# Kernel optimization log

Measured on AMD Instinct MI355X. Metric: run time of the kernel, lower is better.

The kernel has to match this reference:

```python
import jax, jax.numpy as jnp
import numpy as np

BN_EPS = 1e-5
LEAKY_SLOPE = 0.2


def setup_inputs() -> dict:
    key = jax.random.key(0)
    k1, k2 = jax.random.split(key, 2)
    B, C, N, O, K = 8, 64, 4096, 64, 20
    x = jax.random.normal(k1, (B, C, N), dtype=jnp.float32)
    W = jax.random.normal(k2, (O, 2 * C), dtype=jnp.float32) * 0.05  # 1x1 conv weight
    gamma = jnp.ones((O,), dtype=jnp.float32)
    beta = jnp.zeros((O,), dtype=jnp.float32)
    return {"x": x, "W": W, "gamma": gamma, "beta": beta, "k": K}


def reference(x, W, gamma, beta, k):
    # x: (B, C, N)
    xt = jnp.transpose(x, (0, 2, 1))  # (B, N, C)
    # kNN via squared euclidean distances (same ordering as cdist p=2)
    sq = jnp.sum(xt * xt, axis=-1)  # (B, N)
    d2 = sq[:, :, None] + sq[:, None, :] - 2.0 * jnp.einsum('bnc,bmc->bnm', xt, xt)
    idx = jax.lax.top_k(-d2, k)[1]  # (B, N, k) nearest neighbors (incl. self)
    # gather neighbor features: (B, N, k, C)
    xj = jax.vmap(lambda f, i: f[i])(xt, idx)
    xi = xt[:, :, None, :]  # (B, N, 1, C)
    edge = jnp.concatenate([xj - xi, jnp.broadcast_to(xi, xj.shape)], axis=-1)  # (B, N, k, 2C)
    # 1x1 conv == channel GEMM
    h = jnp.einsum('bnkc,oc->bnko', edge, W)  # (B, N, k, O)
    # BatchNorm2d, training-mode batch statistics over (B, N, k) per channel
    mean = jnp.mean(h, axis=(0, 1, 2))
    var = jnp.mean(jnp.square(h - mean), axis=(0, 1, 2))
    hn = (h - mean) * jax.lax.rsqrt(var + BN_EPS) * gamma + beta
    # LeakyReLU(0.2); dropout omitted (eval / identity)
    act = jnp.where(hn >= 0, hn, LEAKY_SLOPE * hn)
    # max over the k neighbors -> (B, N, O) -> (B, O, N)
    out = jnp.max(act, axis=2)
    return jnp.transpose(out, (0, 2, 1))
```

## Files before the change

### kernel.cpp

```cpp
#include <hip/hip_runtime.h>
#include <math.h>

#define Bn 8
#define Cc 64
#define Nn 4096
#define Oo 64
#define Kk 20
#define Kh 10
#define QCAP 16
#define NTOT (Bn*Nn*Kk)

typedef __attribute__((ext_vector_type(8))) short short8;
typedef __attribute__((ext_vector_type(4))) float f32x4;

__device__ __forceinline__ unsigned bf16_rn(float v) {
  unsigned u = __float_as_uint(v);
  return (u + 0x7FFFu + ((u >> 16) & 1)) >> 16;
}

__device__ __forceinline__ float pair_swap_f(float v) {
  return __int_as_float(__builtin_amdgcn_mov_dpp(__float_as_int(v), 0xB1, 0xF, 0xF, true));
}
__device__ __forceinline__ int pair_swap_i(int v) {
  return __builtin_amdgcn_mov_dpp(v, 0xB1, 0xF, 0xF, true);
}

__global__ __launch_bounds__(256) void k_split(const float* __restrict__ x,
                                               unsigned short* __restrict__ xs3,
                                               float* __restrict__ sqv) {
  __shared__ float xs[64][68];
  int tid = threadIdx.x;
  int b = blockIdx.x & 7;
  int n0 = (blockIdx.x >> 3) << 6;
  for (int i = 0; i < 4; i++) {
    int c = i * 16 + (tid >> 4);
    int n = (tid & 15) * 4;
    float4 v = *(const float4*)&x[((size_t)b * Cc + c) * Nn + n0 + n];
    *(float4*)&xs[c][n] = v;
  }
  __syncthreads();
  for (int i = 0; i < 4; i++) {
    int n = i * 16 + (tid >> 4);
    int c = (tid & 15) * 4;
    ushort4 h4, m4, l4;
    unsigned short* hp = (unsigned short*)&h4;
    unsigned short* mp = (unsigned short*)&m4;
    unsigned short* lp = (unsigned short*)&l4;
#pragma unroll
    for (int j = 0; j < 4; j++) {
      float v = xs[c + j][n];
      unsigned hb = bf16_rn(v);
      float hf = __uint_as_float(hb << 16);
      float r1 = v - hf;
      unsigned mb = bf16_rn(r1);
      float mf = __uint_as_float(mb << 16);
      float r2 = r1 - mf;
      unsigned lb = bf16_rn(r2);
      hp[j] = (unsigned short)hb;
      mp[j] = (unsigned short)mb;
      lp[j] = (unsigned short)lb;
    }
    size_t o = ((size_t)(b << 12) + n0 + n) * 192 + c;
    *(ushort4*)&xs3[o] = h4;
    *(ushort4*)&xs3[o + 64] = m4;
    *(ushort4*)&xs3[o + 128] = l4;
  }
  if (tid < 64) {
    float s = 0.f;
#pragma unroll
    for (int c = 0; c < 64; c++) { float v = xs[c][tid]; s = fmaf(v, v, s); }
    sqv[b * Nn + n0 + tid] = s;
  }
}

__global__ __launch_bounds__(256) void k_y1z(const float* __restrict__ x,
                                             const float* __restrict__ Wm,
                                             float* __restrict__ y1,
                                             float* __restrict__ z) {
  __shared__ float xs[64][68];
  __shared__ float Wl[64][129];
  int tid = threadIdx.x;
  int b = blockIdx.x & 7;
  int n0 = (blockIdx.x >> 3) << 6;
  for (int i = tid; i < 64 * 128; i += 256) Wl[i >> 7][i & 127] = Wm[i];
  for (int i = 0; i < 4; i++) {
    int c = i * 16 + (tid >> 4);
    int n = (tid & 15) * 4;
    float4 v = *(const float4*)&x[((size_t)b * Cc + c) * Nn + n0 + n];
    *(float4*)&xs[c][n] = v;
  }
  __syncthreads();
  int o = tid & 63, ng = tid >> 6;
  for (int p = 0; p < 4; p++) {
    int nb = p * 16 + ng * 4;
    float a1[4] = {0.f, 0.f, 0.f, 0.f};
    float a2[4] = {0.f, 0.f, 0.f, 0.f};
#pragma unroll 8
    for (int c = 0; c < 64; c++) {
      float4 xv = *(const float4*)&xs[c][nb];
      float w1v = Wl[o][c], w2v = Wl[o][64 + c];
      float xa[4] = {xv.x, xv.y, xv.z, xv.w};
#pragma unroll
      for (int j = 0; j < 4; j++) {
        a1[j] = fmaf(xa[j], w1v, a1[j]);
        a2[j] = fmaf(xa[j], w2v, a2[j]);
      }
    }
#pragma unroll
    for (int j = 0; j < 4; j++) {
      size_t off = ((size_t)b * Nn + n0 + nb + j) * 64 + o;
      y1[off] = a1[j];
      z[off] = a2[j] - a1[j];
    }
  }
}

__global__ __launch_bounds__(512, 4) void k_knn(const unsigned short* __restrict__ xs3,
                                                const float* __restrict__ sqv,
                                                int* __restrict__ idxout) {
  __shared__ alignas(16) short Bs[2][3][64][72];
  __shared__ float thrS[2][64];
  __shared__ float sqs[2][64];
  __shared__ alignas(16) float qk[2][64][20];
  __shared__ alignas(16) unsigned short qm[2][64][24];
  __shared__ int qcnt[2][64];

  const int tid = threadIdx.x;
  const int lane = tid & 63;
  const int w = tid >> 6;
  const int grp = w >> 2;
  const int wg = w & 3;
  const int tig = tid & 255;
  const int b = blockIdx.x & 7;
  const int n0 = (blockIdx.x >> 3) << 6;
  const int lm = lane & 15;
  const int q = lane >> 4;
  const bool handler = (lane < 32);
  const int hrow = wg * 16 + (lane >> 1);
  const bool isL = (lane & 1) == 0;

  float hk[Kh];
  int hix[Kh];
#pragma unroll
  for (int kk = 0; kk < Kh; kk++) { hk[kk] = INFINITY; hix[kk] = 0; }

  if (handler && !isL) { thrS[grp][hrow] = INFINITY; qcnt[grp][hrow] = 0; }

  const size_t arow = ((size_t)(b << 12) + n0 + wg * 16 + lm) * 192;
  short8 ah0 = *(const short8*)&xs3[arow + q * 8];
  short8 ah1 = *(const short8*)&xs3[arow + 32 + q * 8];
  short8 am0 = *(const short8*)&xs3[arow + 64 + q * 8];
  short8 am1 = *(const short8*)&xs3[arow + 96 + q * 8];
  short8 al0 = *(const short8*)&xs3[arow + 128 + q * 8];
  short8 al1 = *(const short8*)&xs3[arow + 160 + q * 8];

  const unsigned short* gp = xs3 + ((size_t)(b << 12) + grp * 2048) * 192 + tig * 8;
  short* ld[6];
#pragma unroll
  for (int i = 0; i < 6; i++) {
    int f = i * 256 + tig;
    int r = f / 24;
    int rem = f - r * 24;
    int layer = rem >> 3;
    int qq = rem & 7;
    ld[i] = &Bs[grp][layer][r][qq * 8];
  }

  f32x4 acc[4];

  for (int t = 0; t < 32; t++) {
    const int m0 = grp * 2048 + t * 64;
    __syncthreads();
#pragma unroll
    for (int i = 0; i < 6; i++) {
      short8 v = *(const short8*)(gp + i * 2048);
      *(short8*)ld[i] = v;
    }
    gp += 12288;
    if (tig < 16) ((float4*)sqs[grp])[tig] = ((const float4*)(sqv + b * Nn + m0))[tig];
    __syncthreads();

#pragma unroll
    for (int g = 0; g < 4; g++) {
      const int mr = g * 16 + lm;
      short8 bh0 = *(const short8*)&Bs[grp][0][mr][q * 8];
      short8 bh1 = *(const short8*)&Bs[grp][0][mr][32 + q * 8];
      short8 bm0 = *(const short8*)&Bs[grp][1][mr][q * 8];
      short8 bm1 = *(const short8*)&Bs[grp][1][mr][32 + q * 8];
      short8 bl0 = *(const short8*)&Bs[grp][2][mr][q * 8];
      short8 bl1 = *(const short8*)&Bs[grp][2][mr][32 + q * 8];
      f32x4 a = (f32x4){0.f, 0.f, 0.f, 0.f};
      a = __builtin_amdgcn_mfma_f32_16x16x32_bf16(am0, bm0, a, 0, 0, 0);
      a = __builtin_amdgcn_mfma_f32_16x16x32_bf16(am1, bm1, a, 0, 0, 0);
      a = __builtin_amdgcn_mfma_f32_16x16x32_bf16(ah0, bl0, a, 0, 0, 0);
      a = __builtin_amdgcn_mfma_f32_16x16x32_bf16(ah1, bl1, a, 0, 0, 0);
      a = __builtin_amdgcn_mfma_f32_16x16x32_bf16(al0, bh0, a, 0, 0, 0);
      a = __builtin_amdgcn_mfma_f32_16x16x32_bf16(al1, bh1, a, 0, 0, 0);
      a = __builtin_amdgcn_mfma_f32_16x16x32_bf16(ah0, bm0, a, 0, 0, 0);
      a = __builtin_amdgcn_mfma_f32_16x16x32_bf16(ah1, bm1, a, 0, 0, 0);
      a = __builtin_amdgcn_mfma_f32_16x16x32_bf16(am0, bh0, a, 0, 0, 0);
      a = __builtin_amdgcn_mfma_f32_16x16x32_bf16(am1, bh1, a, 0, 0, 0);
      a = __builtin_amdgcn_mfma_f32_16x16x32_bf16(ah0, bh0, a, 0, 0, 0);
      a = __builtin_amdgcn_mfma_f32_16x16x32_bf16(ah1, bh1, a, 0, 0, 0);
      acc[g] = a;
    }

    unsigned pend = 0;
    {
      float tl[4];
#pragma unroll
      for (int r = 0; r < 4; r++) tl[r] = thrS[grp][wg * 16 + q * 4 + r];
      if (grp) {
#pragma unroll
        for (int r = 0; r < 4; r++) tl[r] = fminf(tl[r], thrS[0][wg * 16 + q * 4 + r]);
      }
#pragma unroll
      for (int g = 0; g < 4; g++) {
        float sv = sqs[grp][g * 16 + lm];
#pragma unroll
        for (int r = 0; r < 4; r++) {
          float key = fmaf(-2.f, acc[g][r], sv);
          acc[g][r] = key;
          if (key < tl[r]) pend |= 1u << (g * 4 + r);
        }
      }
    }

    for (;;) {
      if (pend) {
#pragma unroll
        for (int g = 0; g < 4; g++) {
#pragma unroll
          for (int r = 0; r < 4; r++) {
            unsigned bit = 1u << (g * 4 + r);
            if (pend & bit) {
              int row = wg * 16 + q * 4 + r;
              int p = atomicAdd(&qcnt[grp][row], 1);
              if (p < QCAP) {
                qk[grp][row][p] = acc[g][r];
                qm[grp][row][p] = (unsigned short)(m0 + g * 16 + lm);
                pend &= ~bit;
              }
            }
          }
        }
      }
      unsigned long long anyovf = __ballot(pend != 0);

      if (handler) {
        int cn = qcnt[grp][hrow];
        if (cn > QCAP) cn = QCAP;
        for (int p0 = 0; p0 < cn; p0 += 2) {
          float2 kv2 = *(const float2*)&qk[grp][hrow][p0];
          ushort2 mv2 = *(const ushort2*)&qm[grp][hrow][p0];
          float kva[2] = {kv2.x, kv2.y};
          unsigned short mva[2] = {mv2.x, mv2.y};
#pragma unroll
          for (int j = 0; j < 2; j++) {
            bool valid = (p0 + j < cn);
            float kv = kva[j];
            int ki = (int)mva[j];
            bool lins = kv < hk[Kh - 1];
            float pv = lins ? hk[Kh - 1] : kv;
            int pi = lins ? hix[Kh - 1] : ki;
            float rv = pair_swap_f(pv);
            int ri = pair_swap_i(pi);
            float mval = isL ? kv : rv;
            int midx = isL ? ki : ri;
            if (valid && mval < hk[Kh - 1]) {
              bool cm[Kh];
#pragma unroll
              for (int kk = 0; kk < Kh; kk++) cm[kk] = mval < hk[kk];
#pragma unroll
              for (int kk = Kh - 1; kk >= 1; kk--) {
                hk[kk]  = cm[kk] ? (cm[kk - 1] ? hk[kk - 1]  : mval) : hk[kk];
                hix[kk] = cm[kk] ? (cm[kk - 1] ? hix[kk - 1] : midx) : hix[kk];
              }
              if (cm[0]) { hk[0] = mval; hix[0] = midx; }
            }
          }
        }
        if (cn && !isL) { qcnt[grp][hrow] = 0; thrS[grp][hrow] = hk[Kh - 1]; }
      }
      if (!anyovf) break;
      if (pend) {
        float tl[4];
#pragma unroll
        for (int r = 0; r < 4; r++) tl[r] = thrS[grp][wg * 16 + q * 4 + r];
        if (grp) {
#pragma unroll
          for (int r = 0; r < 4; r++) tl[r] = fminf(tl[r], thrS[0][wg * 16 + q * 4 + r]);
        }
#pragma unroll
        for (int g = 0; g < 4; g++)
#pragma unroll
          for (int r = 0; r < 4; r++) {
            unsigned bit = 1u << (g * 4 + r);
            if ((pend & bit) && acc[g][r] >= tl[r]) pend &= ~bit;
          }
      }
    }
  }

  if (grp == 1 && handler) {
    int base = isL ? 0 : Kh;
#pragma unroll
    for (int kk = 0; kk < Kh; kk++) {
      qk[1][hrow][base + kk] = hk[kk];
      qm[1][hrow][base + kk] = (unsigned short)hix[kk];
    }
  }
  __syncthreads();
  if (grp == 0 && handler) {
    for (int p0 = 0; p0 < Kk; p0 += 4) {
      float4 kv4 = *(const float4*)&qk[1][hrow][p0];
      ushort4 mv4 = *(const ushort4*)&qm[1][hrow][p0];
      float kva[4] = {kv4.x, kv4.y, kv4.z, kv4.w};
      unsigned short mva[4] = {mv4.x, mv4.y, mv4.z, mv4.w};
#pragma unroll
      for (int j = 0; j < 4; j++) {
        float kv = kva[j];
        int ki = (int)mva[j];
        bool lins = kv < hk[Kh - 1];
        float pv = lins ? hk[Kh - 1] : kv;
        int pi = lins ? hix[Kh - 1] : ki;
        float rv = pair_swap_f(pv);
        int ri = pair_swap_i(pi);
        float mval = isL ? kv : rv;
        int midx = isL ? ki : ri;
        if (mval < hk[Kh - 1]) {
          bool cm[Kh];
#pragma unroll
          for (int kk = 0; kk < Kh; kk++) cm[kk] = mval < hk[kk];
#pragma unroll
          for (int kk = Kh - 1; kk >= 1; kk--) {
            hk[kk]  = cm[kk] ? (cm[kk - 1] ? hk[kk - 1]  : mval) : hk[kk];
            hix[kk] = cm[kk] ? (cm[kk - 1] ? hix[kk - 1] : midx) : hix[kk];
          }
          if (cm[0]) { hk[0] = mval; hix[0] = midx; }
        }
      }
    }
    size_t obase = ((size_t)b * Nn + n0 + hrow) * Kk + (isL ? 0 : Kh);
#pragma unroll
    for (int kk = 0; kk < Kh; kk++) idxout[obase + kk] = hix[kk];
  }
}

__global__ __launch_bounds__(256) void k_stats(const float* __restrict__ y1,
                                               const float* __restrict__ z,
                                               const int* __restrict__ idxp,
                                               float* __restrict__ parts) {
  __shared__ float rs[4][64];
  __shared__ float rq[4][64];
  int tid = threadIdx.x;
  int o = tid & 63, g = tid >> 6;
  int b = blockIdx.x & 7;
  int n0 = (blockIdx.x >> 3) << 6;
  const float* y1b = y1 + (size_t)b * Nn * 64;
  float s = 0.f, ss = 0.f;
  for (int t = 0; t < 16; t++) {
    int n = n0 + g + t * 4;
    size_t base = (size_t)b * Nn + n;
    float zv = z[base * 64 + o];
    const int* ip = idxp + base * Kk;
#pragma unroll
    for (int k = 0; k < Kk; k++) {
      int j = ip[k];
      float hv = y1b[(size_t)j * 64 + o] + zv;
      s += hv;
      ss = fmaf(hv, hv, ss);
    }
  }
  rs[g][o] = s;
  rq[g][o] = ss;
  __syncthreads();
  if (tid < 64) {
    parts[(size_t)blockIdx.x * 128 + tid] = rs[0][tid] + rs[1][tid] + rs[2][tid] + rs[3][tid];
    parts[(size_t)blockIdx.x * 128 + 64 + tid] = rq[0][tid] + rq[1][tid] + rq[2][tid] + rq[3][tid];
  }
}

__global__ __launch_bounds__(128) void k_reduce(const float* __restrict__ parts,
                                                float* __restrict__ stats) {
  int tid = threadIdx.x;
  float s = 0.f;
  for (int i = 0; i < 512; i += 4) {
    s += parts[(size_t)i * 128 + tid] + parts[(size_t)(i + 1) * 128 + tid] +
         parts[(size_t)(i + 2) * 128 + tid] + parts[(size_t)(i + 3) * 128 + tid];
  }
  stats[tid] = s;
}

__global__ __launch_bounds__(256) void k_out(const float* __restrict__ y1,
                                             const float* __restrict__ z,
                                             const int* __restrict__ idxp,
                                             const float* __restrict__ stats,
                                             const float* __restrict__ gamma,
                                             const float* __restrict__ beta,
                                             float* __restrict__ out) {
  __shared__ float T[64][65];
  int tid = threadIdx.x;
  int lane = tid & 63;
  int w = tid >> 6;
  int b = blockIdx.x & 7;
  int n0 = (blockIdx.x >> 3) << 6;
  int o = lane;
  const float inv = 1.0f / (float)NTOT;
  float mean = stats[o] * inv;
  float var = fmaf(-mean, mean, stats[64 + o] * inv);
  float sc = gamma[o] * rsqrtf(var + 1e-5f);
  float bi = fmaf(-mean, sc, beta[o]);
  const float* y1b = y1 + (size_t)b * Nn * 64;
  for (int t = 0; t < 16; t++) {
    int nl = w + t * 4;
    size_t base = (size_t)b * Nn + n0 + nl;
    float zv = z[base * 64 + o];
    const int* ip = idxp + base * Kk;
    float mv = -INFINITY;
#pragma unroll
    for (int k = 0; k < Kk; k++) {
      int j = ip[k];
      float hv = y1b[(size_t)j * 64 + o] + zv;
      float hn = fmaf(hv, sc, bi);
      float a = (hn >= 0.f) ? hn : 0.2f * hn;
      mv = fmaxf(mv, a);
    }
    T[o][nl] = mv;
  }
  __syncthreads();
  for (int t = 0; t < 16; t++) {
    int oo = w * 16 + t;
    out[((size_t)b * Oo + oo) * Nn + n0 + lane] = T[oo][lane];
  }
}

extern "C" void kernel_launch(void* const* d_in, const int* in_sizes, int n_in,
                              void* d_out, int out_size, void* d_ws, size_t ws_size,
                              hipStream_t stream) {
  const float* x = (const float*)d_in[0];
  const float* W = (const float*)d_in[1];
  const float* gamma = (const float*)d_in[2];
  const float* beta = (const float*)d_in[3];

  char* ws = (char*)d_ws;
  unsigned short* xs3 = (unsigned short*)ws;
  float* y1 = (float*)ws;
  float* z = (float*)(ws + 8388608);
  float* sq = (float*)(ws + 16777216);
  float* stats = (float*)(ws + 16908288);
  int* idx = (int*)(ws + 16908800);
  float* parts = (float*)(ws + 19530240);
  float* out = (float*)d_out;

  k_split<<<Bn * (Nn / 64), 256, 0, stream>>>(x, xs3, sq);
  k_knn<<<Bn * (Nn / 64), 512, 0, stream>>>(xs3, sq, idx);
  k_y1z<<<Bn * (Nn / 64), 256, 0, stream>>>(x, W, y1, z);
  k_stats<<<Bn * (Nn / 64), 256, 0, stream>>>(y1, z, idx, parts);
  k_reduce<<<1, 128, 0, stream>>>(parts, stats);
  k_out<<<Bn * (Nn / 64), 256, 0, stream>>>(y1, z, idx, stats, gamma, beta, out);
}
```

Baseline: 369.8 us.

## Prefetch kNN tiles into registers, swizzle LDS layout, ballot-based queue append

Global loads of the next candidate tile are issued into registers right after the barrier, so they overlap with the MFMA and selection work instead of stalling before the store to LDS. The padded 3D LDS tile becomes a flat XOR-swizzled layout meant to avoid bank conflicts without padding. Shared-memory atomicAdd queue appends are replaced by wave ballot/popcount prefix offsets with per-lane counters, and queue capacity rises to 24. Together these add register pressure and more LDS per block, which may reduce occupancy.

```diff
diff --git a/kernel.cpp b/kernel.cpp
--- a/kernel.cpp
+++ b/kernel.cpp
@@ -7,7 +7,7 @@
 #define Oo 64
 #define Kk 20
 #define Kh 10
-#define QCAP 16
+#define QCAP 24
 #define NTOT (Bn*Nn*Kk)
 
 typedef __attribute__((ext_vector_type(8))) short short8;
@@ -118,11 +118,11 @@
 __global__ __launch_bounds__(512, 4) void k_knn(const unsigned short* __restrict__ xs3,
                                                 const float* __restrict__ sqv,
                                                 int* __restrict__ idxout) {
-  __shared__ alignas(16) short Bs[2][3][64][72];
+  __shared__ alignas(16) short Bs[2][12288];
   __shared__ float thrS[2][64];
   __shared__ float sqs[2][64];
-  __shared__ alignas(16) float qk[2][64][20];
-  __shared__ alignas(16) unsigned short qm[2][64][24];
+  __shared__ alignas(16) float qk[2][64][QCAP];
+  __shared__ alignas(16) unsigned short qm[2][64][QCAP];
   __shared__ int qcnt[2][64];
 
   const int tid = threadIdx.x;
@@ -138,6 +138,10 @@
   const bool handler = (lane < 32);
   const int hrow = wg * 16 + (lane >> 1);
   const bool isL = (lane & 1) == 0;
+  const int rowq = wg * 16 + q * 4;
+
+  const unsigned long long fullseg = 0xFFFFull << (q * 16);
+  const unsigned long long window = ((1ull << lane) - 1) & fullseg;
 
   float hk[Kh];
   int hix[Kh];
@@ -160,35 +164,44 @@
   for (int i = 0; i < 6; i++) {
     int f = i * 256 + tig;
     int r = f / 24;
-    int rem = f - r * 24;
-    int layer = rem >> 3;
-    int qq = rem & 7;
-    ld[i] = &Bs[grp][layer][r][qq * 8];
-  }
+    ld[i] = &Bs[grp][(f * 8) ^ ((r & 7) << 3)];
+  }
+  const int qa = ((q ^ (lm & 7)) << 3);
+  const int qb = (((q + 4) ^ (lm & 7)) << 3);
+  const short* Bg = &Bs[grp][0];
+
+  short8 pv[6];
+#pragma unroll
+  for (int i = 0; i < 6; i++) pv[i] = *(const short8*)(gp + i * 2048);
+  float4 sqpf;
+  if (tig < 16) sqpf = ((const float4*)(sqv + b * Nn + grp * 2048))[tig];
 
   f32x4 acc[4];
+  int qcr[4] = {0, 0, 0, 0};
 
   for (int t = 0; t < 32; t++) {
     const int m0 = grp * 2048 + t * 64;
     __syncthreads();
 #pragma unroll
-    for (int i = 0; i < 6; i++) {
-      short8 v = *(const short8*)(gp + i * 2048);
-      *(short8*)ld[i] = v;
-    }
-    gp += 12288;
-    if (tig < 16) ((float4*)sqs[grp])[tig] = ((const float4*)(sqv + b * Nn + m0))[tig];
+    for (int i = 0; i < 6; i++) *(short8*)ld[i] = pv[i];
+    if (tig < 16) ((float4*)sqs[grp])[tig] = sqpf;
     __syncthreads();
+    if (t < 31) {
+      gp += 12288;
+#pragma unroll
+      for (int i = 0; i < 6; i++) pv[i] = *(const short8*)(gp + i * 2048);
+      if (tig < 16) sqpf = ((const float4*)(sqv + b * Nn + m0 + 64))[tig];
+    }
 
 #pragma unroll
     for (int g = 0; g < 4; g++) {
-      const int mr = g * 16 + lm;
-      short8 bh0 = *(const short8*)&Bs[grp][0][mr][q * 8];
-      short8 bh1 = *(const short8*)&Bs[grp][0][mr][32 + q * 8];
-      short8 bm0 = *(const short8*)&Bs[grp][1][mr][q * 8];
-      short8 bm1 = *(const short8*)&Bs[grp][1][mr][32 + q * 8];
-      short8 bl0 = *(const short8*)&Bs[grp][2][mr][q * 8];
-      short8 bl1 = *(const short8*)&Bs[grp][2][mr][32 + q * 8];
+      const short* brow = Bg + (g * 16 + lm) * 192;
+      short8 bh0 = *(const short8*)(brow + qa);
+      short8 bh1 = *(const short8*)(brow + qb);
+      short8 bm0 = *(const short8*)(brow + 64 + qa);
+      short8 bm1 = *(const short8*)(brow + 64 + qb);
+      short8 bl0 = *(const short8*)(brow + 128 + qa);
+      short8 bl1 = *(const short8*)(brow + 128 + qb);
       f32x4 a = (f32x4){0.f, 0.f, 0.f, 0.f};
       a = __builtin_amdgcn_mfma_f32_16x16x32_bf16(am0, bm0, a, 0, 0, 0);
       a = __builtin_amdgcn_mfma_f32_16x16x32_bf16(am1, bm1, a, 0, 0, 0);
@@ -227,29 +240,38 @@
     }
 
     for (;;) {
-      if (pend) {
+      unsigned long long havep = __ballot(pend != 0);
+      if (havep) {
 #pragma unroll
         for (int g = 0; g < 4; g++) {
 #pragma unroll
           for (int r = 0; r < 4; r++) {
-            unsigned bit = 1u << (g * 4 + r);
-            if (pend & bit) {
-              int row = wg * 16 + q * 4 + r;
-              int p = atomicAdd(&qcnt[grp][row], 1);
-              if (p < QCAP) {
-                qk[grp][row][p] = acc[g][r];
-                qm[grp][row][p] = (unsigned short)(m0 + g * 16 + lm);
-                pend &= ~bit;
-              }
+            const unsigned bit = 1u << (g * 4 + r);
+            bool want = (pend & bit) != 0;
+            unsigned long long mask = __ballot(want);
+            int cnt = (int)__builtin_popcountll(mask & fullseg);
+            int off = (int)__builtin_popcountll(mask & window);
+            int p = qcr[r] + off;
+            if (want && p < QCAP) {
+              qk[grp][rowq + r][p] = acc[g][r];
+              qm[grp][rowq + r][p] = (unsigned short)(m0 + g * 16 + lm);
+              pend &= ~bit;
             }
+            int nq = qcr[r] + cnt;
+            qcr[r] = nq > QCAP ? QCAP : nq;
           }
+        }
+        if (lm == 0) {
+          qcnt[grp][rowq + 0] = qcr[0];
+          qcnt[grp][rowq + 1] = qcr[1];
+          qcnt[grp][rowq + 2] = qcr[2];
+          qcnt[grp][rowq + 3] = qcr[3];
         }
       }
       unsigned long long anyovf = __ballot(pend != 0);
 
       if (handler) {
         int cn = qcnt[grp][hrow];
-        if (cn > QCAP) cn = QCAP;
         for (int p0 = 0; p0 < cn; p0 += 2) {
           float2 kv2 = *(const float2*)&qk[grp][hrow][p0];
           ushort2 mv2 = *(const ushort2*)&qm[grp][hrow][p0];
@@ -261,10 +283,10 @@
             float kv = kva[j];
             int ki = (int)mva[j];
             bool lins = kv < hk[Kh - 1];
-            float pv = lins ? hk[Kh - 1] : kv;
-            int pi = lins ? hix[Kh - 1] : ki;
-            float rv = pair_swap_f(pv);
-            int ri = pair_swap_i(pi);
+            float pv_ = lins ? hk[Kh - 1] : kv;
+            int pi_ = lins ? hix[Kh - 1] : ki;
+            float rv = pair_swap_f(pv_);
+            int ri = pair_swap_i(pi_);
             float mval = isL ? kv : rv;
             int midx = isL ? ki : ri;
             if (valid && mval < hk[Kh - 1]) {
@@ -282,6 +304,7 @@
         }
         if (cn && !isL) { qcnt[grp][hrow] = 0; thrS[grp][hrow] = hk[Kh - 1]; }
       }
+      qcr[0] = 0; qcr[1] = 0; qcr[2] = 0; qcr[3] = 0;
       if (!anyovf) break;
       if (pend) {
         float tl[4];
@@ -318,14 +341,14 @@
       float kva[4] = {kv4.x, kv4.y, kv4.z, kv4.w};
       unsigned short mva[4] = {mv4.x, mv4.y, mv4.z, mv4.w};
 #pragma unroll
-      for (int j = 0; j < 4; j++) {
+    for (int j = 0; j < 4; j++) {
         float kv = kva[j];
         int ki = (int)mva[j];
         bool lins = kv < hk[Kh - 1];
-        float pv = lins ? hk[Kh - 1] : kv;
-        int pi = lins ? hix[Kh - 1] : ki;
-        float rv = pair_swap_f(pv);
-        int ri = pair_swap_i(pi);
+        float pv_ = lins ? hk[Kh - 1] : kv;
+        int pi_ = lins ? hix[Kh - 1] : ki;
+        float rv = pair_swap_f(pv_);
+        int ri = pair_swap_i(pi_);
         float mval = isL ? kv : rv;
         int midx = isL ? ki : ri;
         if (mval < hk[Kh - 1]) {
```

Result: slower. 410.0 us (+10.9%).
